# Kernel tuning notes

Measured on AMD Instinct MI355X. Metric: run time of the kernel, lower is better.

The kernel has to match this reference:

```python
import jax, jax.numpy as jnp
import numpy as np

DIM = 128
HEADS = 4
DIM_HEAD = 32
BASE_SCALE = DIM_HEAD ** (-0.5)
EPS = 1e-5


def _ln(x, g, b):
    mu = jnp.mean(x, axis=-1, keepdims=True)
    var = jnp.mean((x - mu) ** 2, axis=-1, keepdims=True)
    return (x - mu) * jax.lax.rsqrt(var + EPS) * g + b


def setup_inputs() -> dict:
    key = jax.random.key(0)
    ks = jax.random.split(key, 16)
    B, N, X, Y, W1, W2, D = 2, 4, 16, 16, 8, 8, DIM
    C = HEADS * DIM_HEAD
    inp = {
        "q": jax.random.normal(ks[0], (B, N, X, Y, W1, W2, D), jnp.float32),
        "k": jax.random.normal(ks[1], (B, N, X, Y, W1, W2, D), jnp.float32),
        "v": jax.random.normal(ks[2], (B, N, X, Y, W1, W2, D), jnp.float32),
        "skip": jax.random.normal(ks[3], (B, X, Y, W1, W2, D), jnp.float32),
        # per-batch temperature in [0.5, 1.5) to avoid divide blowup
        "temperature": jax.random.uniform(ks[4], (B,), jnp.float32) + 0.5,
        "ln_q_g": jnp.ones((D,), jnp.float32),
        "ln_q_b": jnp.zeros((D,), jnp.float32),
        "ln_k_g": jnp.ones((D,), jnp.float32),
        "ln_k_b": jnp.zeros((D,), jnp.float32),
        "ln_v_g": jnp.ones((D,), jnp.float32),
        "ln_v_b": jnp.zeros((D,), jnp.float32),
        "wq": jax.random.normal(ks[5], (D, C), jnp.float32) * 0.02,
        "bq": jnp.zeros((C,), jnp.float32),
        "wk": jax.random.normal(ks[6], (D, C), jnp.float32) * 0.02,
        "bk": jnp.zeros((C,), jnp.float32),
        "wv": jax.random.normal(ks[7], (D, C), jnp.float32) * 0.02,
        "bv": jnp.zeros((C,), jnp.float32),
        "w_proj": jax.random.normal(ks[8], (C, D), jnp.float32) * 0.02,
        "b_proj": jnp.zeros((D,), jnp.float32),
    }
    return inp


def reference(q, k, v, skip, temperature,
              ln_q_g, ln_q_b, ln_k_g, ln_k_b, ln_v_g, ln_v_b,
              wq, bq, wk, bk, wv, bv, w_proj, b_proj):
    B, N, X, Y, W1, W2, D = q.shape
    L, T = X * Y, N * W1 * W2
    M, Dh = HEADS, DIM_HEAD

    def to_tokens(x):  # b n x y w1 w2 d -> b (x y) (n w1 w2) d
        return jnp.transpose(x, (0, 2, 3, 1, 4, 5, 6)).reshape(B, L, T, D)

    def proj_in(x, g, bb, W, bias):
        return _ln(to_tokens(x), g, bb) @ W + bias  # (B, L, T, M*Dh)

    def split_heads(x):  # channel index = m*Dh + d, heads slow
        return jnp.transpose(x.reshape(B, L, T, M, Dh), (0, 3, 1, 2, 4))  # (B,M,L,T,Dh)

    qh = split_heads(proj_in(q, ln_q_g, ln_q_b, wq, bq))
    kh = split_heads(proj_in(k, ln_k_g, ln_k_b, wk, bk))
    vh = split_heads(proj_in(v, ln_v_g, ln_v_b, wv, bv))

    scale = (BASE_SCALE / temperature)[:, None, None, None, None]  # per-batch, bcast over heads
    dot = jnp.einsum('bmlqd,bmlkd->bmlqk', qh * scale, kh)
    att = jax.nn.softmax(dot, axis=-1)
    a = jnp.einsum('bmlqk,bmlkd->bmlqd', att, vh)  # (B,M,L,T,Dh)

    a = jnp.transpose(a, (0, 2, 3, 1, 4)).reshape(B, L, T, M * Dh)
    a = a.reshape(B, X, Y, N, W1, W2, M * Dh)
    a = jnp.transpose(a, (0, 3, 1, 2, 4, 5, 6))  # b n x y w1 w2 c
    z = a @ w_proj + b_proj
    z = jnp.mean(z, axis=1)  # mean over views n
    return z + skip
```

## Files before the change

### kernel.cpp

```cpp
#include <hip/hip_runtime.h>


typedef unsigned short u16;
typedef short bf16x8 __attribute__((ext_vector_type(8)));
typedef float f32x4 __attribute__((ext_vector_type(4)));

__device__ __forceinline__ float bf2f(u16 u) {
  union { unsigned int i; float f; } v; v.i = ((unsigned int)u) << 16; return v.f;
}
__device__ __forceinline__ u16 f2bf(float f) {
  union { float f; unsigned int i; } v; v.f = f;
  unsigned int x = v.i;
  return (u16)((x + 0x7fffu + ((x >> 16) & 1u)) >> 16);
}

__global__ __launch_bounds__(256) void ln_proj_mfma(
    const float* __restrict__ xq, const float* __restrict__ xk, const float* __restrict__ xv,
    const float* __restrict__ g_q, const float* __restrict__ b_q,
    const float* __restrict__ g_k, const float* __restrict__ b_k,
    const float* __restrict__ g_v, const float* __restrict__ b_v,
    const float* __restrict__ wq, const float* __restrict__ bq,
    const float* __restrict__ wk, const float* __restrict__ bk,
    const float* __restrict__ wv, const float* __restrict__ bv,
    u16* __restrict__ Qp, u16* __restrict__ Kp, u16* __restrict__ Vp)
{
  __shared__ u16 Wt_s[128 * 128];
  __shared__ u16 Y_s[64 * 128];

  const float *xp, *gp, *bp, *Wp, *biasp;
  u16* outp;
  if (blockIdx.y == 0)      { xp = xq; gp = g_q; bp = b_q; Wp = wq; biasp = bq; outp = Qp; }
  else if (blockIdx.y == 1) { xp = xk; gp = g_k; bp = b_k; Wp = wk; biasp = bk; outp = Kp; }
  else                      { xp = xv; gp = g_v; bp = b_v; Wp = wv; biasp = bv; outp = Vp; }

  const int tid = threadIdx.x;

#pragma unroll
  for (int it = 0; it < 16; ++it) {
    int f = it * 256 + tid;
    int d = f >> 5, c4 = (f & 31) * 4;
    float4 w4 = *(const float4*)(Wp + d * 128 + c4);
    Wt_s[(c4 + 0) * 128 + (d ^ (((c4 + 0) & 7) << 3))] = f2bf(w4.x);
    Wt_s[(c4 + 1) * 128 + (d ^ (((c4 + 1) & 7) << 3))] = f2bf(w4.y);
    Wt_s[(c4 + 2) * 128 + (d ^ (((c4 + 2) & 7) << 3))] = f2bf(w4.z);
    Wt_s[(c4 + 3) * 128 + (d ^ (((c4 + 3) & 7) << 3))] = f2bf(w4.w);
  }

  const int lane = tid & 63, wv_ = tid >> 6;
  const int l32 = lane & 31, hi = lane >> 5;
  const int d4 = l32 * 4;
  const float4 g4  = *(const float4*)(gp + d4);
  const float4 bb4 = *(const float4*)(bp + d4);
  const int c0 = lane & 15, g = lane >> 4;

  __syncthreads();

  for (int ci = 0; ci < 8; ++ci) {
    const int tile = blockIdx.x * 8 + ci;
    const int tok0 = tile * 64;
#pragma unroll
    for (int p = 0; p < 8; ++p) {
      int tt = p * 8 + wv_ * 2 + hi;
      int tok = tok0 + tt;
      int t = tok & 255, bl = tok >> 8;
      int l = bl & 255, bi = bl >> 8;
      int xx = l >> 4, yy = l & 15;
      int n = t >> 6, w1 = (t >> 3) & 7, w2 = t & 7;
      int row = (((((bi * 4 + n) * 16 + xx) * 16 + yy) * 8 + w1) * 8 + w2) * 128;
      float4 x4 = *(const float4*)(xp + row + d4);
      float s1 = x4.x + x4.y + x4.z + x4.w;
      float s2 = x4.x * x4.x + x4.y * x4.y + x4.z * x4.z + x4.w * x4.w;
#pragma unroll
      for (int off = 16; off >= 1; off >>= 1) {
        s1 += __shfl_xor(s1, off);
        s2 += __shfl_xor(s2, off);
      }
      float mu = s1 * (1.0f / 128.0f);
      float var = s2 * (1.0f / 128.0f) - mu * mu;
      float rs = rsqrtf(var + 1e-5f);
      ushort4 yv;
      yv.x = f2bf((x4.x - mu) * rs * g4.x + bb4.x);
      yv.y = f2bf((x4.y - mu) * rs * g4.y + bb4.y);
      yv.z = f2bf((x4.z - mu) * rs * g4.z + bb4.z);
      yv.w = f2bf((x4.w - mu) * rs * g4.w + bb4.w);
      *(ushort4*)&Y_s[tt * 128 + (d4 ^ ((tt & 7) << 3))] = yv;
    }
    __syncthreads();
    bf16x8 bfr[4];
#pragma unroll
    for (int ks = 0; ks < 4; ++ks)
      bfr[ks] = *(const bf16x8*)&Y_s[(wv_ * 16 + c0) * 128 + ((ks * 32 + g * 8) ^ ((c0 & 7) << 3))];
#pragma unroll
    for (int ct = 0; ct < 8; ++ct) {
      f32x4 acc = {0.f, 0.f, 0.f, 0.f};
#pragma unroll
      for (int ks = 0; ks < 4; ++ks) {
        bf16x8 afr = *(const bf16x8*)&Wt_s[(ct * 16 + c0) * 128 + ((ks * 32 + g * 8) ^ ((c0 & 7) << 3))];
        acc = __builtin_amdgcn_mfma_f32_16x16x32_bf16(afr, bfr[ks], acc, 0, 0, 0);
      }
      int cb = ct * 16 + g * 4;
      float4 b4 = *(const float4*)(biasp + cb);
      ushort4 zv;
      zv.x = f2bf(acc[0] + b4.x);
      zv.y = f2bf(acc[1] + b4.y);
      zv.z = f2bf(acc[2] + b4.z);
      zv.w = f2bf(acc[3] + b4.w);
      *(ushort4*)(outp + (tok0 + wv_ * 16 + c0) * 128 + cb) = zv;
    }
    __syncthreads();
  }
}

__global__ __launch_bounds__(256) void attn_mfma(
    u16* __restrict__ Qp, const u16* __restrict__ Kp, const u16* __restrict__ Vp,
    const float* __restrict__ temperature)
{
  __shared__ u16 K_s[256 * 32];
  __shared__ u16 Vt_s[32 * 256];
  __shared__ u16 P_s[4][16 * 256];

  const int tid = threadIdx.x;
  const int bid = blockIdx.x;
  const int l = bid & 255, m = (bid >> 8) & 3, b = bid >> 10;
  const float scale = 0.17677669529663689f / temperature[b];
  const int base = (b * 256 + l) * 32768 + m * 32;

#pragma unroll
  for (int r = 0; r < 8; ++r) {
    int f = r * 256 + tid, t = f >> 3, c4 = (f & 7) * 4;
    *(ushort4*)&K_s[t * 32 + c4] = *(const ushort4*)(Kp + base + t * 128 + c4);
  }
  {
    const int dh = tid & 31, kq = tid >> 5;
#pragma unroll
    for (int jj = 0; jj < 4; ++jj) {
      bf16x8 v;
#pragma unroll
      for (int e = 0; e < 8; ++e)
        v[e] = (short)Vp[base + (kq * 32 + jj * 8 + e) * 128 + dh];
      *(bf16x8*)&Vt_s[dh * 256 + ((kq * 32 + jj * 8) ^ ((dh & 7) << 3))] = v;
    }
  }
  __syncthreads();

  const int lane = tid & 63, wv_ = tid >> 6;
  const int c0 = lane & 15, g = lane >> 4;
  u16* Pw = P_s[wv_];
  const f32x4 zero = {0.f, 0.f, 0.f, 0.f};

  for (int si = 0; si < 4; ++si) {
    const int qs = wv_ * 4 + si;
    bf16x8 qf = *(const bf16x8*)(Qp + base + (qs * 16 + c0) * 128 + g * 8);
    f32x4 s[16];
#pragma unroll
    for (int kt = 0; kt < 16; ++kt) {
      bf16x8 kf = *(const bf16x8*)&K_s[(kt * 16 + c0) * 32 + g * 8];
      s[kt] = __builtin_amdgcn_mfma_f32_16x16x32_bf16(qf, kf, zero, 0, 0, 0);
    }
    float p0 = 0.f, p1 = 0.f, p2 = 0.f, p3 = 0.f;
#pragma unroll
    for (int kt = 0; kt < 16; ++kt) {
      float e0 = __expf(s[kt][0] * scale);
      float e1 = __expf(s[kt][1] * scale);
      float e2 = __expf(s[kt][2] * scale);
      float e3 = __expf(s[kt][3] * scale);
      p0 += e0; p1 += e1; p2 += e2; p3 += e3;
      int col = kt * 16 + c0;
      int r0 = g * 4;
      Pw[(r0 + 0) * 256 + (col ^ (((r0 + 0) & 7) << 3))] = f2bf(e0);
      Pw[(r0 + 1) * 256 + (col ^ (((r0 + 1) & 7) << 3))] = f2bf(e1);
      Pw[(r0 + 2) * 256 + (col ^ (((r0 + 2) & 7) << 3))] = f2bf(e2);
      Pw[(r0 + 3) * 256 + (col ^ (((r0 + 3) & 7) << 3))] = f2bf(e3);
    }
#pragma unroll
    for (int off = 1; off <= 8; off <<= 1) {
      p0 += __shfl_xor(p0, off);
      p1 += __shfl_xor(p1, off);
      p2 += __shfl_xor(p2, off);
      p3 += __shfl_xor(p3, off);
    }
    float inv0 = 1.0f / p0, inv1 = 1.0f / p1, inv2 = 1.0f / p2, inv3 = 1.0f / p3;
    f32x4 o0 = zero, o1 = zero;
#pragma unroll
    for (int kc = 0; kc < 8; ++kc) {
      int off8 = (kc * 32 + g * 8) ^ ((c0 & 7) << 3);
      bf16x8 af = *(const bf16x8*)&Pw[c0 * 256 + off8];
      bf16x8 v0 = *(const bf16x8*)&Vt_s[c0 * 256 + off8];
      bf16x8 v1 = *(const bf16x8*)&Vt_s[(16 + c0) * 256 + off8];
      o0 = __builtin_amdgcn_mfma_f32_16x16x32_bf16(af, v0, o0, 0, 0, 0);
      o1 = __builtin_amdgcn_mfma_f32_16x16x32_bf16(af, v1, o1, 0, 0, 0);
    }
    int qrow = qs * 16 + g * 4;
    Qp[base + (qrow + 0) * 128 + c0]      = f2bf(o0[0] * inv0);
    Qp[base + (qrow + 1) * 128 + c0]      = f2bf(o0[1] * inv1);
    Qp[base + (qrow + 2) * 128 + c0]      = f2bf(o0[2] * inv2);
    Qp[base + (qrow + 3) * 128 + c0]      = f2bf(o0[3] * inv3);
    Qp[base + (qrow + 0) * 128 + 16 + c0] = f2bf(o1[0] * inv0);
    Qp[base + (qrow + 1) * 128 + 16 + c0] = f2bf(o1[1] * inv1);
    Qp[base + (qrow + 2) * 128 + 16 + c0] = f2bf(o1[2] * inv2);
    Qp[base + (qrow + 3) * 128 + 16 + c0] = f2bf(o1[3] * inv3);
  }
}

__global__ __launch_bounds__(256) void out_proj_kernel(
    const u16* __restrict__ Ap, const float* __restrict__ wp, const float* __restrict__ bpr,
    const float* __restrict__ skip, float* __restrict__ out, int chunks_per_block)
{
  __shared__ u16   WP_s[128 * 128];
  __shared__ float a_s[128][8];
  const int tid = threadIdx.x;
#pragma unroll
  for (int r = 0; r < 16; ++r) {
    int f4 = r * 256 + tid;
    float4 w4 = *(const float4*)(wp + f4 * 4);
    ushort4 u; u.x = f2bf(w4.x); u.y = f2bf(w4.y); u.z = f2bf(w4.z); u.w = f2bf(w4.w);
    *(ushort4*)&WP_s[f4 * 4] = u;
  }
  const int pp = tid >> 7, c = tid & 127;
  const float bias_c = bpr[c];
  const int tj = tid & 7, cb = (tid >> 3) * 4;
  __syncthreads();

  for (int ci = 0; ci < chunks_per_block; ++ci) {
    const int ch = blockIdx.x * chunks_per_block + ci;
    {
      int o = ch * 8 + tj;
      int w = o & 63, bl = o >> 6;
      int l = bl & 255, b = bl >> 8;
      int rb = (b * 256 + l) * 32768;
      float4 sum = make_float4(0.f, 0.f, 0.f, 0.f);
#pragma unroll
      for (int n = 0; n < 4; ++n) {
        int t = n * 64 + w;
        ushort4 a4 = *(const ushort4*)(Ap + rb + t * 128 + cb);
        sum.x += bf2f(a4.x); sum.y += bf2f(a4.y);
        sum.z += bf2f(a4.z); sum.w += bf2f(a4.w);
      }
      a_s[cb + 0][tj] = sum.x; a_s[cb + 1][tj] = sum.y;
      a_s[cb + 2][tj] = sum.z; a_s[cb + 3][tj] = sum.w;
    }
    __syncthreads();
    {
      float a0 = 0, a1 = 0, a2 = 0, a3 = 0;
#pragma unroll 4
      for (int cp = 0; cp < 128; ++cp) {
        float4 av = *(const float4*)&a_s[cp][pp * 4];
        float w = bf2f(WP_s[cp * 128 + c]);
        a0 += av.x * w; a1 += av.y * w; a2 += av.z * w; a3 += av.w * w;
      }
      int ob = (ch * 8 + pp * 4) * 128 + c;
      out[ob]       = 0.25f * a0 + bias_c + skip[ob];
      out[ob + 128] = 0.25f * a1 + bias_c + skip[ob + 128];
      out[ob + 256] = 0.25f * a2 + bias_c + skip[ob + 256];
      out[ob + 384] = 0.25f * a3 + bias_c + skip[ob + 384];
    }
    __syncthreads();
  }
}

extern "C" void kernel_launch(void* const* d_in, const int* in_sizes, int n_in,
                              void* d_out, int out_size, void* d_ws, size_t ws_size,
                              hipStream_t stream)
{
  (void)in_sizes; (void)n_in; (void)out_size; (void)ws_size;
  const float* q    = (const float*)d_in[0];
  const float* k    = (const float*)d_in[1];
  const float* v    = (const float*)d_in[2];
  const float* skip = (const float*)d_in[3];
  const float* temp = (const float*)d_in[4];
  const float* gq   = (const float*)d_in[5];
  const float* bq_l = (const float*)d_in[6];
  const float* gk   = (const float*)d_in[7];
  const float* bk_l = (const float*)d_in[8];
  const float* gv   = (const float*)d_in[9];
  const float* bv_l = (const float*)d_in[10];
  const float* wq   = (const float*)d_in[11];
  const float* bq   = (const float*)d_in[12];
  const float* wk   = (const float*)d_in[13];
  const float* bk   = (const float*)d_in[14];
  const float* wv   = (const float*)d_in[15];
  const float* bv   = (const float*)d_in[16];
  const float* wp   = (const float*)d_in[17];
  const float* bp   = (const float*)d_in[18];
  float* out = (float*)d_out;

  const size_t S = (size_t)2 * 256 * 256 * 128;
  u16* Qp = (u16*)d_ws;
  u16* Kp = Qp + S;
  u16* Vp = Kp + S;

  ln_proj_mfma<<<dim3(256, 3), 256, 0, stream>>>(
      q, k, v, gq, bq_l, gk, bk_l, gv, bv_l,
      wq, bq, wk, bk, wv, bv, Qp, Kp, Vp);
  attn_mfma<<<dim3(2048), 256, 0, stream>>>(Qp, Kp, Vp, temp);
  out_proj_kernel<<<dim3(512), 256, 0, stream>>>(Qp, wp, bp, skip, out, 8);
}
```

Baseline: 376.6 us.

## Fold LayerNorm into projection GEMM, pre-transpose V, chunk attention, MFMA out-proj

The LN+projection kernel now folds gamma into the weights. It applies the mean/rstd correction after the MFMA using precomputed column sums, so raw inputs feed the GEMM directly from registers with no LDS staging. V is written head-transposed so the attention kernel loads it with coalesced vectors instead of strided scalar gathers. Attention processes keys in 64-wide chunks to shrink the P buffer and register use. The output projection is rebuilt on MFMA with the view-mean folded into the weights. Inputs are now quantised to bf16 before normalisation, and V is stored with scattered 2-byte writes, which may cost accuracy and write bandwidth.

```diff
diff --git a/kernel.cpp b/kernel.cpp
--- a/kernel.cpp
+++ b/kernel.cpp
@@ -2,6 +2,7 @@
 
 
 typedef unsigned short u16;
+typedef unsigned int u32;
 typedef short bf16x8 __attribute__((ext_vector_type(8)));
 typedef float f32x4 __attribute__((ext_vector_type(4)));
 
@@ -22,124 +23,142 @@
     const float* __restrict__ wq, const float* __restrict__ bq,
     const float* __restrict__ wk, const float* __restrict__ bk,
     const float* __restrict__ wv, const float* __restrict__ bv,
-    u16* __restrict__ Qp, u16* __restrict__ Kp, u16* __restrict__ Vp)
+    u16* __restrict__ Qp, u16* __restrict__ Kp, u16* __restrict__ VpT)
 {
-  __shared__ u16 Wt_s[128 * 128];
-  __shared__ u16 Y_s[64 * 128];
+  __shared__ u16  Wt_s[128 * 136];
+  __shared__ float S_s[128];
+  __shared__ float B2_s[128];
 
   const float *xp, *gp, *bp, *Wp, *biasp;
   u16* outp;
   if (blockIdx.y == 0)      { xp = xq; gp = g_q; bp = b_q; Wp = wq; biasp = bq; outp = Qp; }
   else if (blockIdx.y == 1) { xp = xk; gp = g_k; bp = b_k; Wp = wk; biasp = bk; outp = Kp; }
-  else                      { xp = xv; gp = g_v; bp = b_v; Wp = wv; biasp = bv; outp = Vp; }
+  else                      { xp = xv; gp = g_v; bp = b_v; Wp = wv; biasp = bv; outp = VpT; }
 
   const int tid = threadIdx.x;
 
 #pragma unroll
-  for (int it = 0; it < 16; ++it) {
+  for (int it = 0; it < 32; ++it) {
     int f = it * 256 + tid;
-    int d = f >> 5, c4 = (f & 31) * 4;
-    float4 w4 = *(const float4*)(Wp + d * 128 + c4);
-    Wt_s[(c4 + 0) * 128 + (d ^ (((c4 + 0) & 7) << 3))] = f2bf(w4.x);
-    Wt_s[(c4 + 1) * 128 + (d ^ (((c4 + 1) & 7) << 3))] = f2bf(w4.y);
-    Wt_s[(c4 + 2) * 128 + (d ^ (((c4 + 2) & 7) << 3))] = f2bf(w4.z);
-    Wt_s[(c4 + 3) * 128 + (d ^ (((c4 + 3) & 7) << 3))] = f2bf(w4.w);
-  }
+    int c = f & 127, d0 = (f >> 7) * 2;
+    float w0 = Wp[d0 * 128 + c] * gp[d0];
+    float w1 = Wp[(d0 + 1) * 128 + c] * gp[d0 + 1];
+    u32 pk = (u32)f2bf(w0) | ((u32)f2bf(w1) << 16);
+    *(u32*)&Wt_s[c * 136 + (d0 ^ ((c & 15) << 3))] = pk;
+  }
+  {
+    int c = tid & 127;
+    float accv = 0.f;
+#pragma unroll 4
+    for (int d = 0; d < 128; ++d) {
+      float coef = (tid < 128) ? gp[d] : bp[d];
+      accv += coef * Wp[d * 128 + c];
+    }
+    if (tid < 128) S_s[c] = accv;
+    else           B2_s[c] = accv + biasp[c];
+  }
+  __syncthreads();
 
   const int lane = tid & 63, wv_ = tid >> 6;
-  const int l32 = lane & 31, hi = lane >> 5;
-  const int d4 = l32 * 4;
-  const float4 g4  = *(const float4*)(gp + d4);
-  const float4 bb4 = *(const float4*)(bp + d4);
   const int c0 = lane & 15, g = lane >> 4;
 
-  __syncthreads();
-
-  for (int ci = 0; ci < 8; ++ci) {
-    const int tile = blockIdx.x * 8 + ci;
-    const int tok0 = tile * 64;
-#pragma unroll
-    for (int p = 0; p < 8; ++p) {
-      int tt = p * 8 + wv_ * 2 + hi;
-      int tok = tok0 + tt;
-      int t = tok & 255, bl = tok >> 8;
+  for (int rnd = 0; rnd < 4; ++rnd) {
+    const int tilebase = (blockIdx.x * 4 + rnd) * 2;
+    bf16x8 xf[2][4];
+    float mu[2], rsv[2];
+    int tokv[2];
+#pragma unroll
+    for (int t = 0; t < 2; ++t) {
+      int tok = (tilebase + t) * 64 + wv_ * 16 + c0;
+      tokv[t] = tok;
+      int tt = tok & 255, bl = tok >> 8;
       int l = bl & 255, bi = bl >> 8;
       int xx = l >> 4, yy = l & 15;
-      int n = t >> 6, w1 = (t >> 3) & 7, w2 = t & 7;
+      int n = tt >> 6, w1 = (tt >> 3) & 7, w2 = tt & 7;
       int row = (((((bi * 4 + n) * 16 + xx) * 16 + yy) * 8 + w1) * 8 + w2) * 128;
-      float4 x4 = *(const float4*)(xp + row + d4);
-      float s1 = x4.x + x4.y + x4.z + x4.w;
-      float s2 = x4.x * x4.x + x4.y * x4.y + x4.z * x4.z + x4.w * x4.w;
-#pragma unroll
-      for (int off = 16; off >= 1; off >>= 1) {
-        s1 += __shfl_xor(s1, off);
-        s2 += __shfl_xor(s2, off);
-      }
-      float mu = s1 * (1.0f / 128.0f);
-      float var = s2 * (1.0f / 128.0f) - mu * mu;
-      float rs = rsqrtf(var + 1e-5f);
-      ushort4 yv;
-      yv.x = f2bf((x4.x - mu) * rs * g4.x + bb4.x);
-      yv.y = f2bf((x4.y - mu) * rs * g4.y + bb4.y);
-      yv.z = f2bf((x4.z - mu) * rs * g4.z + bb4.z);
-      yv.w = f2bf((x4.w - mu) * rs * g4.w + bb4.w);
-      *(ushort4*)&Y_s[tt * 128 + (d4 ^ ((tt & 7) << 3))] = yv;
-    }
-    __syncthreads();
-    bf16x8 bfr[4];
-#pragma unroll
-    for (int ks = 0; ks < 4; ++ks)
-      bfr[ks] = *(const bf16x8*)&Y_s[(wv_ * 16 + c0) * 128 + ((ks * 32 + g * 8) ^ ((c0 & 7) << 3))];
+      float s1 = 0.f, s2 = 0.f;
+#pragma unroll
+      for (int ks = 0; ks < 4; ++ks) {
+        float4 lo = *(const float4*)(xp + row + ks * 32 + g * 8);
+        float4 hi = *(const float4*)(xp + row + ks * 32 + g * 8 + 4);
+        s1 += lo.x + lo.y + lo.z + lo.w + hi.x + hi.y + hi.z + hi.w;
+        s2 += lo.x * lo.x + lo.y * lo.y + lo.z * lo.z + lo.w * lo.w
+            + hi.x * hi.x + hi.y * hi.y + hi.z * hi.z + hi.w * hi.w;
+        bf16x8 xv;
+        xv[0] = (short)f2bf(lo.x); xv[1] = (short)f2bf(lo.y);
+        xv[2] = (short)f2bf(lo.z); xv[3] = (short)f2bf(lo.w);
+        xv[4] = (short)f2bf(hi.x); xv[5] = (short)f2bf(hi.y);
+        xv[6] = (short)f2bf(hi.z); xv[7] = (short)f2bf(hi.w);
+        xf[t][ks] = xv;
+      }
+      s1 += __shfl_xor(s1, 16); s2 += __shfl_xor(s2, 16);
+      s1 += __shfl_xor(s1, 32); s2 += __shfl_xor(s2, 32);
+      float m = s1 * (1.0f / 128.0f);
+      float var = s2 * (1.0f / 128.0f) - m * m;
+      mu[t] = m;
+      rsv[t] = rsqrtf(var + 1e-5f);
+    }
 #pragma unroll
     for (int ct = 0; ct < 8; ++ct) {
-      f32x4 acc = {0.f, 0.f, 0.f, 0.f};
-#pragma unroll
-      for (int ks = 0; ks < 4; ++ks) {
-        bf16x8 afr = *(const bf16x8*)&Wt_s[(ct * 16 + c0) * 128 + ((ks * 32 + g * 8) ^ ((c0 & 7) << 3))];
-        acc = __builtin_amdgcn_mfma_f32_16x16x32_bf16(afr, bfr[ks], acc, 0, 0, 0);
-      }
-      int cb = ct * 16 + g * 4;
-      float4 b4 = *(const float4*)(biasp + cb);
-      ushort4 zv;
-      zv.x = f2bf(acc[0] + b4.x);
-      zv.y = f2bf(acc[1] + b4.y);
-      zv.z = f2bf(acc[2] + b4.z);
-      zv.w = f2bf(acc[3] + b4.w);
-      *(ushort4*)(outp + (tok0 + wv_ * 16 + c0) * 128 + cb) = zv;
-    }
-    __syncthreads();
+      const int cb = ct * 16 + g * 4;
+      float4 S4 = *(const float4*)&S_s[cb];
+      float4 B4 = *(const float4*)&B2_s[cb];
+      bf16x8 wf[4];
+#pragma unroll
+      for (int ks = 0; ks < 4; ++ks)
+        wf[ks] = *(const bf16x8*)&Wt_s[(ct * 16 + c0) * 136 + ((ks * 32 + g * 8) ^ (c0 << 3))];
+#pragma unroll
+      for (int t = 0; t < 2; ++t) {
+        f32x4 acc = {0.f, 0.f, 0.f, 0.f};
+#pragma unroll
+        for (int ks = 0; ks < 4; ++ks)
+          acc = __builtin_amdgcn_mfma_f32_16x16x32_bf16(wf[ks], xf[t][ks], acc, 0, 0, 0);
+        float z0 = rsv[t] * (acc[0] - mu[t] * S4.x) + B4.x;
+        float z1 = rsv[t] * (acc[1] - mu[t] * S4.y) + B4.y;
+        float z2 = rsv[t] * (acc[2] - mu[t] * S4.z) + B4.z;
+        float z3 = rsv[t] * (acc[3] - mu[t] * S4.w) + B4.w;
+        if (blockIdx.y == 2) {
+          int head = (tokv[t] >> 8) * 4 + (cb >> 5);
+          int dh0 = cb & 31, tcol = tokv[t] & 255;
+          outp[(head * 32 + dh0 + 0) * 256 + tcol] = f2bf(z0);
+          outp[(head * 32 + dh0 + 1) * 256 + tcol] = f2bf(z1);
+          outp[(head * 32 + dh0 + 2) * 256 + tcol] = f2bf(z2);
+          outp[(head * 32 + dh0 + 3) * 256 + tcol] = f2bf(z3);
+        } else {
+          ushort4 zv;
+          zv.x = f2bf(z0); zv.y = f2bf(z1); zv.z = f2bf(z2); zv.w = f2bf(z3);
+          *(ushort4*)(outp + tokv[t] * 128 + cb) = zv;
+        }
+      }
+    }
   }
 }
 
 __global__ __launch_bounds__(256) void attn_mfma(
-    u16* __restrict__ Qp, const u16* __restrict__ Kp, const u16* __restrict__ Vp,
+    u16* __restrict__ Qp, const u16* __restrict__ Kp, const u16* __restrict__ VpT,
     const float* __restrict__ temperature)
 {
   __shared__ u16 K_s[256 * 32];
   __shared__ u16 Vt_s[32 * 256];
-  __shared__ u16 P_s[4][16 * 256];
+  __shared__ u16 P_s[4][16 * 64];
 
   const int tid = threadIdx.x;
   const int bid = blockIdx.x;
   const int l = bid & 255, m = (bid >> 8) & 3, b = bid >> 10;
   const float scale = 0.17677669529663689f / temperature[b];
   const int base = (b * 256 + l) * 32768 + m * 32;
+  const int head = (b * 256 + l) * 4 + m;
 
 #pragma unroll
   for (int r = 0; r < 8; ++r) {
     int f = r * 256 + tid, t = f >> 3, c4 = (f & 7) * 4;
     *(ushort4*)&K_s[t * 32 + c4] = *(const ushort4*)(Kp + base + t * 128 + c4);
   }
-  {
-    const int dh = tid & 31, kq = tid >> 5;
-#pragma unroll
-    for (int jj = 0; jj < 4; ++jj) {
-      bf16x8 v;
-#pragma unroll
-      for (int e = 0; e < 8; ++e)
-        v[e] = (short)Vp[base + (kq * 32 + jj * 8 + e) * 128 + dh];
-      *(bf16x8*)&Vt_s[dh * 256 + ((kq * 32 + jj * 8) ^ ((dh & 7) << 3))] = v;
-    }
+#pragma unroll
+  for (int r = 0; r < 8; ++r) {
+    int f = r * 256 + tid, dh = f >> 6, c4 = (f & 63) * 4;
+    ushort4 vv = *(const ushort4*)(VpT + (head * 32 + dh) * 256 + c4);
+    *(ushort4*)&Vt_s[dh * 256 + (c4 ^ ((dh & 7) << 3))] = vv;
   }
   __syncthreads();
 
@@ -151,26 +170,39 @@
   for (int si = 0; si < 4; ++si) {
     const int qs = wv_ * 4 + si;
     bf16x8 qf = *(const bf16x8*)(Qp + base + (qs * 16 + c0) * 128 + g * 8);
-    f32x4 s[16];
-#pragma unroll
-    for (int kt = 0; kt < 16; ++kt) {
-      bf16x8 kf = *(const bf16x8*)&K_s[(kt * 16 + c0) * 32 + g * 8];
-      s[kt] = __builtin_amdgcn_mfma_f32_16x16x32_bf16(qf, kf, zero, 0, 0, 0);
-    }
     float p0 = 0.f, p1 = 0.f, p2 = 0.f, p3 = 0.f;
-#pragma unroll
-    for (int kt = 0; kt < 16; ++kt) {
-      float e0 = __expf(s[kt][0] * scale);
-      float e1 = __expf(s[kt][1] * scale);
-      float e2 = __expf(s[kt][2] * scale);
-      float e3 = __expf(s[kt][3] * scale);
-      p0 += e0; p1 += e1; p2 += e2; p3 += e3;
-      int col = kt * 16 + c0;
-      int r0 = g * 4;
-      Pw[(r0 + 0) * 256 + (col ^ (((r0 + 0) & 7) << 3))] = f2bf(e0);
-      Pw[(r0 + 1) * 256 + (col ^ (((r0 + 1) & 7) << 3))] = f2bf(e1);
-      Pw[(r0 + 2) * 256 + (col ^ (((r0 + 2) & 7) << 3))] = f2bf(e2);
-      Pw[(r0 + 3) * 256 + (col ^ (((r0 + 3) & 7) << 3))] = f2bf(e3);
+    f32x4 o0 = zero, o1 = zero;
+    const int r0 = g * 4;
+#pragma unroll 1
+    for (int cc = 0; cc < 4; ++cc) {
+      f32x4 s[4];
+#pragma unroll
+      for (int kt = 0; kt < 4; ++kt) {
+        bf16x8 kf = *(const bf16x8*)&K_s[((cc * 4 + kt) * 16 + c0) * 32 + g * 8];
+        s[kt] = __builtin_amdgcn_mfma_f32_16x16x32_bf16(qf, kf, zero, 0, 0, 0);
+      }
+#pragma unroll
+      for (int kt = 0; kt < 4; ++kt) {
+        float e0 = __expf(s[kt][0] * scale);
+        float e1 = __expf(s[kt][1] * scale);
+        float e2 = __expf(s[kt][2] * scale);
+        float e3 = __expf(s[kt][3] * scale);
+        p0 += e0; p1 += e1; p2 += e2; p3 += e3;
+        int col = kt * 16 + c0;
+        Pw[(r0 + 0) * 64 + (col ^ (((r0 + 0) & 7) << 3))] = f2bf(e0);
+        Pw[(r0 + 1) * 64 + (col ^ (((r0 + 1) & 7) << 3))] = f2bf(e1);
+        Pw[(r0 + 2) * 64 + (col ^ (((r0 + 2) & 7) << 3))] = f2bf(e2);
+        Pw[(r0 + 3) * 64 + (col ^ (((r0 + 3) & 7) << 3))] = f2bf(e3);
+      }
+#pragma unroll
+      for (int kc = 0; kc < 2; ++kc) {
+        bf16x8 af = *(const bf16x8*)&Pw[c0 * 64 + ((kc * 32 + g * 8) ^ ((c0 & 7) << 3))];
+        int Kg = cc * 64 + kc * 32 + g * 8;
+        bf16x8 v0 = *(const bf16x8*)&Vt_s[c0 * 256 + (Kg ^ ((c0 & 7) << 3))];
+        bf16x8 v1 = *(const bf16x8*)&Vt_s[(16 + c0) * 256 + (Kg ^ ((c0 & 7) << 3))];
+        o0 = __builtin_amdgcn_mfma_f32_16x16x32_bf16(af, v0, o0, 0, 0, 0);
+        o1 = __builtin_amdgcn_mfma_f32_16x16x32_bf16(af, v1, o1, 0, 0, 0);
+      }
     }
 #pragma unroll
     for (int off = 1; off <= 8; off <<= 1) {
@@ -180,16 +212,6 @@
       p3 += __shfl_xor(p3, off);
     }
     float inv0 = 1.0f / p0, inv1 = 1.0f / p1, inv2 = 1.0f / p2, inv3 = 1.0f / p3;
-    f32x4 o0 = zero, o1 = zero;
-#pragma unroll
-    for (int kc = 0; kc < 8; ++kc) {
-      int off8 = (kc * 32 + g * 8) ^ ((c0 & 7) << 3);
-      bf16x8 af = *(const bf16x8*)&Pw[c0 * 256 + off8];
-      bf16x8 v0 = *(const bf16x8*)&Vt_s[c0 * 256 + off8];
-      bf16x8 v1 = *(const bf16x8*)&Vt_s[(16 + c0) * 256 + off8];
-      o0 = __builtin_amdgcn_mfma_f32_16x16x32_bf16(af, v0, o0, 0, 0, 0);
-      o1 = __builtin_amdgcn_mfma_f32_16x16x32_bf16(af, v1, o1, 0, 0, 0);
-    }
     int qrow = qs * 16 + g * 4;
     Qp[base + (qrow + 0) * 128 + c0]      = f2bf(o0[0] * inv0);
     Qp[base + (qrow + 1) * 128 + c0]      = f2bf(o0[1] * inv1);
@@ -202,59 +224,62 @@
   }
 }
 
-__global__ __launch_bounds__(256) void out_proj_kernel(
+__global__ __launch_bounds__(256) void out_proj_mfma(
     const u16* __restrict__ Ap, const float* __restrict__ wp, const float* __restrict__ bpr,
-    const float* __restrict__ skip, float* __restrict__ out, int chunks_per_block)
+    const float* __restrict__ skip, float* __restrict__ out)
 {
-  __shared__ u16   WP_s[128 * 128];
-  __shared__ float a_s[128][8];
+  __shared__ u16 WpT_s[128 * 136];
   const int tid = threadIdx.x;
 #pragma unroll
-  for (int r = 0; r < 16; ++r) {
-    int f4 = r * 256 + tid;
-    float4 w4 = *(const float4*)(wp + f4 * 4);
-    ushort4 u; u.x = f2bf(w4.x); u.y = f2bf(w4.y); u.z = f2bf(w4.z); u.w = f2bf(w4.w);
-    *(ushort4*)&WP_s[f4 * 4] = u;
-  }
-  const int pp = tid >> 7, c = tid & 127;
-  const float bias_c = bpr[c];
-  const int tj = tid & 7, cb = (tid >> 3) * 4;
+  for (int it = 0; it < 32; ++it) {
+    int f = it * 256 + tid;
+    int c = f & 127, d0 = (f >> 7) * 2;
+    float w0 = wp[d0 * 128 + c] * 0.25f;
+    float w1 = wp[(d0 + 1) * 128 + c] * 0.25f;
+    u32 pk = (u32)f2bf(w0) | ((u32)f2bf(w1) << 16);
+    *(u32*)&WpT_s[c * 136 + (d0 ^ ((c & 15) << 3))] = pk;
+  }
   __syncthreads();
 
-  for (int ci = 0; ci < chunks_per_block; ++ci) {
-    const int ch = blockIdx.x * chunks_per_block + ci;
-    {
-      int o = ch * 8 + tj;
-      int w = o & 63, bl = o >> 6;
-      int l = bl & 255, b = bl >> 8;
-      int rb = (b * 256 + l) * 32768;
-      float4 sum = make_float4(0.f, 0.f, 0.f, 0.f);
-#pragma unroll
-      for (int n = 0; n < 4; ++n) {
-        int t = n * 64 + w;
-        ushort4 a4 = *(const ushort4*)(Ap + rb + t * 128 + cb);
-        sum.x += bf2f(a4.x); sum.y += bf2f(a4.y);
-        sum.z += bf2f(a4.z); sum.w += bf2f(a4.w);
-      }
-      a_s[cb + 0][tj] = sum.x; a_s[cb + 1][tj] = sum.y;
-      a_s[cb + 2][tj] = sum.z; a_s[cb + 3][tj] = sum.w;
-    }
-    __syncthreads();
-    {
-      float a0 = 0, a1 = 0, a2 = 0, a3 = 0;
-#pragma unroll 4
-      for (int cp = 0; cp < 128; ++cp) {
-        float4 av = *(const float4*)&a_s[cp][pp * 4];
-        float w = bf2f(WP_s[cp * 128 + c]);
-        a0 += av.x * w; a1 += av.y * w; a2 += av.z * w; a3 += av.w * w;
-      }
-      int ob = (ch * 8 + pp * 4) * 128 + c;
-      out[ob]       = 0.25f * a0 + bias_c + skip[ob];
-      out[ob + 128] = 0.25f * a1 + bias_c + skip[ob + 128];
-      out[ob + 256] = 0.25f * a2 + bias_c + skip[ob + 256];
-      out[ob + 384] = 0.25f * a3 + bias_c + skip[ob + 384];
-    }
-    __syncthreads();
+  const int lane = tid & 63, wv_ = tid >> 6;
+  const int c0 = lane & 15, g = lane >> 4;
+  const int bl = blockIdx.x;
+  const int w = wv_ * 16 + c0;
+  const int otok = bl * 64 + w;
+
+  bf16x8 bfr[4];
+#pragma unroll
+  for (int ks = 0; ks < 4; ++ks) {
+    float acc8[8] = {0.f, 0.f, 0.f, 0.f, 0.f, 0.f, 0.f, 0.f};
+#pragma unroll
+    for (int n = 0; n < 4; ++n) {
+      bf16x8 a = *(const bf16x8*)(Ap + (bl * 256 + n * 64 + w) * 128 + ks * 32 + g * 8);
+#pragma unroll
+      for (int e = 0; e < 8; ++e) acc8[e] += bf2f((u16)a[e]);
+    }
+    bf16x8 r;
+#pragma unroll
+    for (int e = 0; e < 8; ++e) r[e] = (short)f2bf(acc8[e]);
+    bfr[ks] = r;
+  }
+#pragma unroll
+  for (int ct = 0; ct < 8; ++ct) {
+    f32x4 acc = {0.f, 0.f, 0.f, 0.f};
+#pragma unroll
+    for (int ks = 0; ks < 4; ++ks) {
+      bf16x8 wf = *(const bf16x8*)&WpT_s[(ct * 16 + c0) * 136 + ((ks * 32 + g * 8) ^ (c0 << 3))];
+      acc = __builtin_amdgcn_mfma_f32_16x16x32_bf16(wf, bfr[ks], acc, 0, 0, 0);
+    }
+    int d0 = ct * 16 + g * 4;
+    int ob = otok * 128 + d0;
+    float4 sk = *(const float4*)(skip + ob);
+    float4 b4 = *(const float4*)(bpr + d0);
+    float4 zv;
+    zv.x = acc[0] + b4.x + sk.x;
+    zv.y = acc[1] + b4.y + sk.y;
+    zv.z = acc[2] + b4.z + sk.z;
+    zv.w = acc[3] + b4.w + sk.w;
+    *(float4*)(out + ob) = zv;
   }
 }
 
@@ -285,13 +310,13 @@
   float* out = (float*)d_out;
 
   const size_t S = (size_t)2 * 256 * 256 * 128;
-  u16* Qp = (u16*)d_ws;
-  u16* Kp = Qp + S;
-  u16* Vp = Kp + S;
+  u16* Qp  = (u16*)d_ws;
+  u16* Kp  = Qp + S;
+  u16* VpT = Kp + S;
 
   ln_proj_mfma<<<dim3(256, 3), 256, 0, stream>>>(
       q, k, v, gq, bq_l, gk, bk_l, gv, bv_l,
-      wq, bq, wk, bk, wv, bv, Qp, Kp, Vp);
-  attn_mfma<<<dim3(2048), 256, 0, stream>>>(Qp, Kp, Vp, temp);
-  out_proj_kernel<<<dim3(512), 256, 0, stream>>>(Qp, wp, bp, skip, out, 8);
-}
+      wq, bq, wk, bk, wv, bv, Qp, Kp, VpT);
+  attn_mfma<<<dim3(2048), 256, 0, stream>>>(Qp, Kp, VpT, temp);
+  out_proj_mfma<<<dim3(512), 256, 0, stream>>>(Qp, wp, bp, skip, out);
+}
```

Measured after the change: 348.8 us. 1.08x faster.
